# Kernel optimization log

Measured on AMD Instinct MI355X. Metric: run time of the kernel, lower is better.

## Reference

```python
import jax, jax.numpy as jnp
import numpy as np

N = 20000
E = 320000
H = 16
C = 16
NUM_GRAPHS = 64
NEG_SLOPE = 0.2


def _gat(x, edge_index, W, a_src, a_dst, bias):
    # PyG GATConv, concat=True, shared lin for src/dst, eval mode (no dropout)
    h = (x @ W).reshape(-1, H, C)                       # [N,H,C]
    src, dst = edge_index[0], edge_index[1]
    alpha_src = jnp.sum(h * a_src, axis=-1)             # [N,H]
    alpha_dst = jnp.sum(h * a_dst, axis=-1)             # [N,H]
    alpha = alpha_src[src] + alpha_dst[dst]             # [E,H]
    alpha = jax.nn.leaky_relu(alpha, NEG_SLOPE)
    amax = jax.ops.segment_max(alpha, dst, num_segments=N)
    ex = jnp.exp(alpha - amax[dst])
    denom = jax.ops.segment_sum(ex, dst, num_segments=N)
    attn = ex / jnp.where(denom == 0, 1.0, denom)[dst]  # [E,H]
    msg = h[src] * attn[:, :, None]                     # [E,H,C]
    out = jax.ops.segment_sum(msg, dst, num_segments=N) # [N,H,C]
    return out.reshape(-1, H * C) + bias


def setup_inputs() -> dict:
    key = jax.random.key(0)
    ks = jax.random.split(key, 32)
    d = {}
    d['x'] = jax.random.normal(ks[0], (N, 20), dtype=jnp.float32)
    d['edge_index_ipv6'] = jax.random.randint(ks[1], (2, E), 0, N)
    d['edge_attr_ipv6'] = jax.random.normal(ks[2], (E, 19), dtype=jnp.float32)
    d['edge_index_tsch'] = jax.random.randint(ks[3], (2, E), 0, N)
    d['edge_attr_tsch'] = jax.random.normal(ks[4], (E, 7), dtype=jnp.float32)
    d['batch'] = jnp.sort(jax.random.randint(ks[5], (N,), 0, NUM_GRAPHS))
    s = 0.1
    d['W_i'] = jax.random.normal(ks[6], (20, H * C), dtype=jnp.float32) * s
    d['a_src_i'] = jax.random.normal(ks[7], (H, C), dtype=jnp.float32) * s
    d['a_dst_i'] = jax.random.normal(ks[8], (H, C), dtype=jnp.float32) * s
    d['b_i'] = jnp.zeros((H * C,), dtype=jnp.float32)
    d['W_t'] = jax.random.normal(ks[9], (20, H * C), dtype=jnp.float32) * s
    d['a_src_t'] = jax.random.normal(ks[10], (H, C), dtype=jnp.float32) * s
    d['a_dst_t'] = jax.random.normal(ks[11], (H, C), dtype=jnp.float32) * s
    d['b_t'] = jnp.zeros((H * C,), dtype=jnp.float32)
    d['Wf'] = jax.random.normal(ks[12], (512, 64), dtype=jnp.float32) * s
    d['bf'] = jnp.zeros((64,), dtype=jnp.float32)
    d['W1'] = jax.random.normal(ks[13], (64, 32), dtype=jnp.float32) * s
    d['b1'] = jnp.zeros((32,), dtype=jnp.float32)
    d['W2'] = jax.random.normal(ks[14], (32, 16), dtype=jnp.float32) * s
    d['b2'] = jnp.zeros((16,), dtype=jnp.float32)
    d['W3'] = jax.random.normal(ks[15], (16, 16), dtype=jnp.float32) * s
    d['b3'] = jnp.zeros((16,), dtype=jnp.float32)
    d['Wce'] = jax.random.normal(ks[16], (16, 3), dtype=jnp.float32) * s
    d['bce'] = jnp.zeros((3,), dtype=jnp.float32)
    d['Wcv'] = jax.random.normal(ks[17], (16, 3), dtype=jnp.float32) * s
    d['bcv'] = jnp.zeros((3,), dtype=jnp.float32)
    return d


def reference(x, edge_index_ipv6, edge_attr_ipv6, edge_index_tsch, edge_attr_tsch,
              batch, W_i, a_src_i, a_dst_i, b_i, W_t, a_src_t, a_dst_t, b_t,
              Wf, bf, W1, b1, W2, b2, W3, b3, Wce, bce, Wcv, bcv):
    # edge_attr_* are ignored by GATConv (edge_dim=None in PyG), as in original
    n_ipv6 = _gat(x, edge_index_ipv6, W_i, a_src_i, a_dst_i, b_i)
    n_tsch = _gat(x, edge_index_tsch, W_t, a_src_t, a_dst_t, b_t)
    h = jnp.concatenate([n_ipv6, n_tsch], axis=-1)      # [N,512]
    h = jax.nn.relu(h @ Wf + bf)
    h = jax.nn.relu(h @ W1 + b1)
    h = jax.nn.relu(h @ W2 + b2)
    h = jax.nn.relu(h @ W3 + b3)                        # [N,16]
    ssum = jax.ops.segment_sum(h, batch, num_segments=NUM_GRAPHS)
    cnt = jax.ops.segment_sum(jnp.ones((h.shape[0], 1), h.dtype), batch,
                              num_segments=NUM_GRAPHS)
    g = ssum / jnp.where(cnt == 0, 1.0, cnt)            # [G,16]
    out_event = g @ Wce + bce
    out_env = g @ Wcv + bcv
    return out_event, out_env
```

## Files before the change

kernel.cpp:

```cpp
#include <hip/hip_runtime.h>
#include <math.h>

#define N_NODES 20000
#define N_EDGES 320000
#define NG 64
#define NEG 0.2f
#define NCHUNK ((N_NODES + 255) / 256)

typedef __attribute__((ext_vector_type(8))) short bf16x8;
typedef __attribute__((ext_vector_type(4))) float f32x4;

__device__ __forceinline__ unsigned short f2bf(float f) {
  unsigned int u = __float_as_uint(f);
  return (unsigned short)((u + 0x7fffu + ((u >> 16) & 1u)) >> 16);
}

__global__ __launch_bounds__(256) void k_prep(
    const float* __restrict__ W_i, const float* __restrict__ as_i, const float* __restrict__ ad_i,
    const float* __restrict__ W_t, const float* __restrict__ as_t, const float* __restrict__ ad_t,
    const float* __restrict__ Wf, const float* __restrict__ bf,
    const float* __restrict__ b_i, const float* __restrict__ b_t,
    float* __restrict__ wsall, unsigned short* __restrict__ wbigfrag,
    float* __restrict__ bfold,
    int* __restrict__ fill_i, int* __restrict__ fill_t,
    float* __restrict__ gsum, int* __restrict__ gcnt) {
  __shared__ float bred[4][64];
  int idx = blockIdx.x * 256 + threadIdx.x;
  if (idx < 1280) {
    int k = idx >> 6, c = idx & 63;
    int set = c >> 5, role = (c >> 4) & 1, h = c & 15;
    const float* W = set ? W_t : W_i;
    const float* a = set ? (role ? ad_t : as_t) : (role ? ad_i : as_i);
    float v = 0.f;
#pragma unroll
    for (int j = 0; j < 16; ++j) v = fmaf(W[k * 256 + h * 16 + j], a[h * 16 + j], v);
    wsall[idx] = v;
    return;
  }
  idx -= 1280;
  if (idx < 49152) {
    int ct = idx / 12288, rem = idx % 12288;
    int lane = (rem >> 3) & 63, j = rem & 7, ks = rem >> 9;
    int k = ks * 32 + ((lane >> 4) << 3) + j;
    int nc = ct * 16 + (lane & 15);
    float v = 0.f;
    int g = (k >= 384) ? 1 : 0;
    int r = k - g * 384;
    int h = r / 24, c = r - h * 24;
    if (c < 20) {
      const float* W = g ? W_t : W_i;
      const float* wr = W + c * 256 + (h << 4);
      const float* wf = Wf + ((g << 8) + (h << 4)) * 64 + nc;
#pragma unroll
      for (int m = 0; m < 16; ++m) v = fmaf(wr[m], wf[m * 64], v);
    }
    wbigfrag[idx] = f2bf(v);
    return;
  }
  idx -= 49152;
  if (idx < 256) {
    int t = threadIdx.x, wv = t >> 6, j = t & 63;
    float p = 0.f;
    int i0 = wv * 128;
#pragma unroll 4
    for (int i = i0; i < i0 + 128; ++i) {
      float b = (i < 256) ? b_i[i] : b_t[i - 256];
      p = fmaf(b, Wf[i * 64 + j], p);
    }
    bred[wv][j] = p;
    __syncthreads();
    if (wv == 0) bfold[j] = bred[0][j] + bred[1][j] + bred[2][j] + bred[3][j] + bf[j];
    return;
  }
  idx -= 256;
  if (idx < N_NODES) { fill_i[idx] = 0; return; }
  idx -= N_NODES;
  if (idx < N_NODES) { fill_t[idx] = 0; return; }
  idx -= N_NODES;
  if (idx < NG * 16) { gsum[idx] = 0.f; return; }
  idx -= NG * 16;
  if (idx < NG) gcnt[idx] = 0;
}

__global__ __launch_bounds__(256) void k_alpha(
    const float* __restrict__ x, const float* __restrict__ wsall,
    float* __restrict__ xpad,
    float* __restrict__ asrc0, float* __restrict__ adst0,
    float* __restrict__ asrc1, float* __restrict__ adst1) {
  int t = threadIdx.x;
  int n0 = blockIdx.x * 16;
  __shared__ float xs[16][20];
  __shared__ float ws[20][64];
  for (int i = t; i < 16 * 20; i += 256) {
    int nd = i / 20, k = i % 20;
    xs[nd][k] = x[(n0 + nd) * 20 + k];
  }
  for (int i = t; i < 1280; i += 256) ws[i >> 6][i & 63] = wsall[i];
  __syncthreads();
  for (int i = t; i < 512; i += 256) {
    int nd = i >> 5, j = i & 31;
    xpad[(size_t)(n0 + nd) * 32 + j] = (j < 20) ? xs[nd][j] : 0.f;
  }
#pragma unroll
  for (int i = 0; i < 4; ++i) {
    int wi = i * 256 + t;
    int nd = wi >> 6, c = wi & 63;
    float v = 0.f;
#pragma unroll
    for (int k = 0; k < 20; ++k) v = fmaf(xs[nd][k], ws[k][c], v);
    int n = n0 + nd, h = c & 15;
    float* arr = (c >> 5) ? ((c >> 4) & 1 ? adst1 : asrc1)
                          : ((c >> 4) & 1 ? adst0 : asrc0);
    arr[n * 16 + h] = v;
  }
}

__global__ void k_hist(const int* __restrict__ ei0, const int* __restrict__ ei1,
                       int* __restrict__ cnt0, int* __restrict__ cnt1) {
  int e = blockIdx.x * blockDim.x + threadIdx.x;
  if (e >= N_EDGES) return;
  if (blockIdx.y == 0)
    atomicAdd(&cnt0[ei0[N_EDGES + e]], 1);
  else
    atomicAdd(&cnt1[ei1[N_EDGES + e]], 1);
}

__global__ __launch_bounds__(256) void k_scan1(
    const int* __restrict__ cnt0, const int* __restrict__ cnt1,
    int* __restrict__ tmp0, int* __restrict__ tmp1, int* __restrict__ csums) {
  int chunk = blockIdx.x, set = blockIdx.y;
  const int* cnt = set ? cnt1 : cnt0;
  int* tmp = set ? tmp1 : tmp0;
  int t = threadIdx.x, lane = t & 63, wv = t >> 6;
  int i = chunk * 256 + t;
  int v = (i < N_NODES) ? cnt[i] : 0;
  int s = v;
#pragma unroll
  for (int d = 1; d < 64; d <<= 1) {
    int o = __shfl_up(s, d);
    if (lane >= d) s += o;
  }
  __shared__ int wsum[4];
  if (lane == 63) wsum[wv] = s;
  __syncthreads();
  int pre = 0;
#pragma unroll
  for (int j = 0; j < 4; ++j)
    if (j < wv) pre += wsum[j];
  s += pre;
  if (i < N_NODES) tmp[i] = s;
  if (t == 255) csums[set * 128 + chunk] = s;
}

__global__ __launch_bounds__(256) void k_scan3(
    const int* __restrict__ tmp0, const int* __restrict__ tmp1,
    const int* __restrict__ csums,
    int* __restrict__ rp0, int* __restrict__ rp1,
    int* __restrict__ fill0, int* __restrict__ fill1) {
  int chunk = blockIdx.x, set = blockIdx.y;
  const int* tmp = set ? tmp1 : tmp0;
  int* rp = set ? rp1 : rp0;
  int* fill = set ? fill1 : fill0;
  __shared__ int soff;
  if (threadIdx.x == 0) {
    int acc = 0;
    for (int cc = 0; cc < chunk; ++cc) acc += csums[set * 128 + cc];
    soff = acc;
  }
  __syncthreads();
  int off = soff;
  int i = chunk * 256 + threadIdx.x;
  if (i >= N_NODES) return;
  int incl = tmp[i];
  int c = fill[i];
  int excl = off + incl - c;
  rp[i] = excl;
  fill[i] = excl;
  if (i == N_NODES - 1) rp[N_NODES] = off + incl;
}

__global__ void k_scatter(const int* __restrict__ ei0, const int* __restrict__ ei1,
                          int* __restrict__ fill0, int* __restrict__ fill1,
                          unsigned short* __restrict__ srcs0,
                          unsigned short* __restrict__ srcs1) {
  int e = blockIdx.x * blockDim.x + threadIdx.x;
  if (e >= N_EDGES) return;
  const int* ei = blockIdx.y ? ei1 : ei0;
  int* fill = blockIdx.y ? fill1 : fill0;
  unsigned short* srcs = blockIdx.y ? srcs1 : srcs0;
  int d = ei[N_EDGES + e];
  int pos = atomicAdd(&fill[d], 1);
  srcs[pos] = (unsigned short)ei[e];
}

__global__ __launch_bounds__(256) void k_gat(
    const float* __restrict__ xpad,
    const float* __restrict__ asrc0, const float* __restrict__ adst0,
    const float* __restrict__ asrc1, const float* __restrict__ adst1,
    const int* __restrict__ rp0, const unsigned short* __restrict__ srcs0,
    const int* __restrict__ rp1, const unsigned short* __restrict__ srcs1,
    unsigned short* __restrict__ xagg) {
  __shared__ float lds[4][416];
  int w4 = threadIdx.x >> 6, lane = threadIdx.x & 63;
  int n = blockIdx.x * 2 + (w4 >> 1);
  int g = w4 & 1;
  int h16 = lane & 15, e4 = lane >> 4;
  float* lxs = lds[w4];
  float* lat = lds[w4] + 288;

  const float* asrc = g ? asrc1 : asrc0;
  const float* adst = g ? adst1 : adst0;
  const int* rp = g ? rp1 : rp0;
  const unsigned short* srcs = g ? srcs1 : srcs0;
  int k0 = rp[n], k1 = rp[n + 1];
  int deg = k1 - k0;
  float adn = adst[n * 16 + h16];
  float lacc = 0.f;
  float xa[8];
#pragma unroll
  for (int j = 0; j < 8; ++j) xa[j] = 0.f;

  if (deg > 0) {
    int nbat = (deg + 7) >> 3;
    int s0a = (int)srcs[min(k0 + e4, k1 - 1)];
    int s0b = (int)srcs[min(k0 + 4 + e4, k1 - 1)];
    float av0a = asrc[s0a * 16 + h16];
    float av0b = asrc[s0b * 16 + h16];
    float2 xv0a = *(const float2*)&xpad[(size_t)s0a * 32 + h16 * 2];
    float2 xv0b = *(const float2*)&xpad[(size_t)s0b * 32 + h16 * 2];
    int s1a = 0, s1b = 0;
    if (nbat > 1) {
      s1a = (int)srcs[min(k0 + 8 + e4, k1 - 1)];
      s1b = (int)srcs[min(k0 + 12 + e4, k1 - 1)];
    }
    for (int bb = 0; bb < nbat; ++bb) {
      float av1a = 0.f, av1b = 0.f;
      float2 xv1a = {0.f, 0.f}, xv1b = {0.f, 0.f};
      int s2a = 0, s2b = 0;
      if (bb + 1 < nbat) {
        av1a = asrc[s1a * 16 + h16];
        av1b = asrc[s1b * 16 + h16];
        xv1a = *(const float2*)&xpad[(size_t)s1a * 32 + h16 * 2];
        xv1b = *(const float2*)&xpad[(size_t)s1b * 32 + h16 * 2];
      }
      if (bb + 2 < nbat) {
        int kb = k0 + (bb + 2) * 8;
        s2a = (int)srcs[min(kb + e4, k1 - 1)];
        s2b = (int)srcs[min(kb + 4 + e4, k1 - 1)];
      }
      int base = k0 + bb * 8;
      float a1 = av0a + adn; a1 = a1 >= 0.f ? a1 : NEG * a1;
      float a2 = av0b + adn; a2 = a2 >= 0.f ? a2 : NEG * a2;
      float exa = (base + e4 < k1) ? __expf(a1) : 0.f;
      float exb = (base + 4 + e4 < k1) ? __expf(a2) : 0.f;
      lacc += exa + exb;
      lat[e4 * 16 + h16] = exa;
      lat[(4 + e4) * 16 + h16] = exb;
      *(float2*)&lxs[e4 * 36 + h16 * 2] = xv0a;
      *(float2*)&lxs[(4 + e4) * 36 + h16 * 2] = xv0b;
#pragma unroll
      for (int e = 0; e < 8; ++e) {
        float w = lat[e * 16 + h16];
        const float4 x0 = *(const float4*)&lxs[e * 36 + e4 * 8];
        const float4 x1 = *(const float4*)&lxs[e * 36 + e4 * 8 + 4];
        xa[0] = fmaf(w, x0.x, xa[0]); xa[1] = fmaf(w, x0.y, xa[1]);
        xa[2] = fmaf(w, x0.z, xa[2]); xa[3] = fmaf(w, x0.w, xa[3]);
        xa[4] = fmaf(w, x1.x, xa[4]); xa[5] = fmaf(w, x1.y, xa[5]);
        xa[6] = fmaf(w, x1.z, xa[6]); xa[7] = fmaf(w, x1.w, xa[7]);
      }
      av0a = av1a; av0b = av1b; xv0a = xv1a; xv0b = xv1b;
      s0a = s1a; s0b = s1b; s1a = s2a; s1b = s2b;
    }
  }
  float lh = lacc + __shfl_xor(lacc, 16);
  lh += __shfl_xor(lh, 32);
  float invl = lh > 0.f ? 1.f / lh : 0.f;
  if (e4 < 3) {
    unsigned int u[4];
#pragma unroll
    for (int q = 0; q < 4; ++q)
      u[q] = (unsigned int)f2bf(xa[2 * q] * invl) |
             ((unsigned int)f2bf(xa[2 * q + 1] * invl) << 16);
    *(uint4*)&xagg[(size_t)n * 768 + g * 384 + h16 * 24 + e4 * 8] = *(uint4*)u;
  }
}

__global__ __launch_bounds__(256) void k_mlp(
    const unsigned short* __restrict__ xagg, const unsigned short* __restrict__ wbigfrag,
    const float* __restrict__ bfold,
    const float* __restrict__ W1m, const float* __restrict__ b1v,
    const float* __restrict__ W2m, const float* __restrict__ b2v,
    const float* __restrict__ W3m, const float* __restrict__ b3v,
    const int* __restrict__ batch,
    float* __restrict__ gsum, int* __restrict__ gcnt) {
  int t = threadIdx.x, w = t >> 6, lane = t & 63;
  int n0 = blockIdx.x * 64;
  __shared__ float o1[64][68];
  __shared__ float o2[64][36];
  __shared__ float o3[64][20];
  __shared__ float o4[64][17];
  __shared__ int bs[64];
  if (t < 64) bs[t] = batch[min(n0 + t, N_NODES - 1)];

  {
    int m = lane & 15, kb = lane >> 4;
    int arow = n0 + w * 16 + m;
    if (arow >= N_NODES) arow = N_NODES - 1;
    const unsigned short* aptr = xagg + (size_t)arow * 768 + kb * 8;
    f32x4 acc0 = {0.f, 0.f, 0.f, 0.f}, acc1 = acc0, acc2 = acc0, acc3 = acc0;
#pragma unroll 4
    for (int ks = 0; ks < 24; ++ks) {
      bf16x8 af = *(const bf16x8*)(aptr + ks * 32);
      const unsigned short* bks = wbigfrag + (size_t)ks * 512 + lane * 8;
      bf16x8 b0 = *(const bf16x8*)(bks);
      bf16x8 b1 = *(const bf16x8*)(bks + 12288);
      bf16x8 b2 = *(const bf16x8*)(bks + 24576);
      bf16x8 b3 = *(const bf16x8*)(bks + 36864);
      acc0 = __builtin_amdgcn_mfma_f32_16x16x32_bf16(af, b0, acc0, 0, 0, 0);
      acc1 = __builtin_amdgcn_mfma_f32_16x16x32_bf16(af, b1, acc1, 0, 0, 0);
      acc2 = __builtin_amdgcn_mfma_f32_16x16x32_bf16(af, b2, acc2, 0, 0, 0);
      acc3 = __builtin_amdgcn_mfma_f32_16x16x32_bf16(af, b3, acc3, 0, 0, 0);
    }
    int col = lane & 15, rg = lane >> 4;
#pragma unroll
    for (int r = 0; r < 4; ++r) {
      int row = w * 16 + rg * 4 + r;
      o1[row][col]      = fmaxf(acc0[r] + bfold[col], 0.f);
      o1[row][16 + col] = fmaxf(acc1[r] + bfold[16 + col], 0.f);
      o1[row][32 + col] = fmaxf(acc2[r] + bfold[32 + col], 0.f);
      o1[row][48 + col] = fmaxf(acc3[r] + bfold[48 + col], 0.f);
    }
  }
  __syncthreads();
  int nd = t >> 2, qo = t & 3;
  {
    float a[8];
#pragma unroll
    for (int j = 0; j < 8; ++j) a[j] = b1v[qo * 8 + j];
#pragma unroll 4
    for (int k = 0; k < 64; ++k) {
      float hv = o1[nd][k];
      const float4 wA = *(const float4*)&W1m[k * 32 + qo * 8];
      const float4 wB = *(const float4*)&W1m[k * 32 + qo * 8 + 4];
      a[0] = fmaf(hv, wA.x, a[0]); a[1] = fmaf(hv, wA.y, a[1]);
      a[2] = fmaf(hv, wA.z, a[2]); a[3] = fmaf(hv, wA.w, a[3]);
      a[4] = fmaf(hv, wB.x, a[4]); a[5] = fmaf(hv, wB.y, a[5]);
      a[6] = fmaf(hv, wB.z, a[6]); a[7] = fmaf(hv, wB.w, a[7]);
    }
#pragma unroll
    for (int j = 0; j < 8; ++j) o2[nd][qo * 8 + j] = fmaxf(a[j], 0.f);
  }
  __syncthreads();
  {
    float a[4];
    const float4 bb = *(const float4*)&b2v[qo * 4];
    a[0] = bb.x; a[1] = bb.y; a[2] = bb.z; a[3] = bb.w;
#pragma unroll 4
    for (int k = 0; k < 32; ++k) {
      float hv = o2[nd][k];
      const float4 ww = *(const float4*)&W2m[k * 16 + qo * 4];
      a[0] = fmaf(hv, ww.x, a[0]); a[1] = fmaf(hv, ww.y, a[1]);
      a[2] = fmaf(hv, ww.z, a[2]); a[3] = fmaf(hv, ww.w, a[3]);
    }
#pragma unroll
    for (int j = 0; j < 4; ++j) o3[nd][qo * 4 + j] = fmaxf(a[j], 0.f);
  }
  __syncthreads();
  {
    float a[4];
    const float4 bb = *(const float4*)&b3v[qo * 4];
    a[0] = bb.x; a[1] = bb.y; a[2] = bb.z; a[3] = bb.w;
#pragma unroll
    for (int k = 0; k < 16; ++k) {
      float hv = o3[nd][k];
      const float4 ww = *(const float4*)&W3m[k * 16 + qo * 4];
      a[0] = fmaf(hv, ww.x, a[0]); a[1] = fmaf(hv, ww.y, a[1]);
      a[2] = fmaf(hv, ww.z, a[2]); a[3] = fmaf(hv, ww.w, a[3]);
    }
#pragma unroll
    for (int j = 0; j < 4; ++j) o4[nd][qo * 4 + j] = fmaxf(a[j], 0.f);
  }
  __syncthreads();
  if (t < 128) {
    int s = t >> 4, js = t & 15;
    int b = bs[0] + s;
    if (b <= bs[63]) {
      float sum = 0.f; int c = 0;
#pragma unroll 8
      for (int ndd = 0; ndd < 64; ++ndd) {
        if (n0 + ndd < N_NODES && bs[ndd] == b) { sum += o4[ndd][js]; ++c; }
      }
      if (c > 0) {
        atomicAdd(&gsum[b * 16 + js], sum);
        if (js == 0) atomicAdd(&gcnt[b], c);
      }
    }
  }
}

__global__ void k_head(const float* __restrict__ gsum, const int* __restrict__ gcnt,
                       const float* __restrict__ Wce, const float* __restrict__ bce,
                       const float* __restrict__ Wcv, const float* __restrict__ bcv,
                       float* __restrict__ out) {
  int t = threadIdx.x;
  if (t >= 384) return;
  int half = t / 192, idx = t % 192;
  int b = idx / 3, r = idx % 3;
  float cnt = (float)gcnt[b];
  float inv = cnt > 0.f ? 1.f / cnt : 1.f;
  const float* Wc = half ? Wcv : Wce;
  const float* bc = half ? bcv : bce;
  float v = bc[r];
#pragma unroll
  for (int j = 0; j < 16; ++j) v = fmaf(gsum[b * 16 + j] * inv, Wc[j * 3 + r], v);
  out[t] = v;
}

extern "C" void kernel_launch(void* const* d_in, const int* in_sizes, int n_in,
                              void* d_out, int out_size, void* d_ws, size_t ws_size,
                              hipStream_t stream) {
  const float* x = (const float*)d_in[0];
  const int* ei_i = (const int*)d_in[1];
  const int* ei_t = (const int*)d_in[3];
  const int* batch = (const int*)d_in[5];
  const float* W_i = (const float*)d_in[6];
  const float* as_i = (const float*)d_in[7];
  const float* ad_i = (const float*)d_in[8];
  const float* b_i = (const float*)d_in[9];
  const float* W_t = (const float*)d_in[10];
  const float* as_t = (const float*)d_in[11];
  const float* ad_t = (const float*)d_in[12];
  const float* b_t = (const float*)d_in[13];
  const float* Wf = (const float*)d_in[14];
  const float* bf = (const float*)d_in[15];
  const float* W1 = (const float*)d_in[16];
  const float* b1 = (const float*)d_in[17];
  const float* W2 = (const float*)d_in[18];
  const float* b2 = (const float*)d_in[19];
  const float* W3 = (const float*)d_in[20];
  const float* b3 = (const float*)d_in[21];
  const float* Wce = (const float*)d_in[22];
  const float* bce = (const float*)d_in[23];
  const float* Wcv = (const float*)d_in[24];
  const float* bcv = (const float*)d_in[25];

  char* ws = (char*)d_ws;
  size_t off = 0;
  auto take = [&](size_t bytes) {
    void* p = ws + off;
    off = (off + bytes + 255) & ~(size_t)255;
    return p;
  };
  float* xpad = (float*)take((size_t)N_NODES * 32 * 4);
  unsigned short* xagg = (unsigned short*)take((size_t)N_NODES * 768 * 2);
  float* wsall = (float*)take((size_t)1280 * 4);
  unsigned short* wbigfrag = (unsigned short*)take((size_t)49152 * 2);
  float* bfold = (float*)take((size_t)64 * 4);
  float* asrc_i = (float*)take((size_t)N_NODES * 16 * 4);
  float* adst_i = (float*)take((size_t)N_NODES * 16 * 4);
  float* asrc_t = (float*)take((size_t)N_NODES * 16 * 4);
  float* adst_t = (float*)take((size_t)N_NODES * 16 * 4);
  int* rowptr_i = (int*)take((size_t)(N_NODES + 1) * 4);
  int* rowptr_t = (int*)take((size_t)(N_NODES + 1) * 4);
  int* fill_i = (int*)take((size_t)N_NODES * 4);
  int* fill_t = (int*)take((size_t)N_NODES * 4);
  int* tmp_i = (int*)take((size_t)N_NODES * 4);
  int* tmp_t = (int*)take((size_t)N_NODES * 4);
  int* csums = (int*)take((size_t)2 * 128 * 4);
  unsigned short* srcs_i = (unsigned short*)take((size_t)N_EDGES * 2);
  unsigned short* srcs_t = (unsigned short*)take((size_t)N_EDGES * 2);
  float* gsum = (float*)take((size_t)NG * 16 * 4);
  int* gcnt = (int*)take((size_t)NG * 4);

  int prep_items = 1280 + 49152 + 256 + N_NODES + N_NODES + NG * 16 + NG;
  k_prep<<<(prep_items + 255) / 256, 256, 0, stream>>>(
      W_i, as_i, ad_i, W_t, as_t, ad_t, Wf, bf, b_i, b_t,
      wsall, wbigfrag, bfold, fill_i, fill_t, gsum, gcnt);

  k_alpha<<<N_NODES / 16, 256, 0, stream>>>(x, wsall, xpad,
                                            asrc_i, adst_i, asrc_t, adst_t);

  dim3 egrid((N_EDGES + 255) / 256, 2);
  k_hist<<<egrid, 256, 0, stream>>>(ei_i, ei_t, fill_i, fill_t);
  dim3 sgrid(NCHUNK, 2);
  k_scan1<<<sgrid, 256, 0, stream>>>(fill_i, fill_t, tmp_i, tmp_t, csums);
  k_scan3<<<sgrid, 256, 0, stream>>>(tmp_i, tmp_t, csums, rowptr_i, rowptr_t,
                                     fill_i, fill_t);
  k_scatter<<<egrid, 256, 0, stream>>>(ei_i, ei_t, fill_i, fill_t, srcs_i, srcs_t);

  k_gat<<<N_NODES / 2, 256, 0, stream>>>(xpad, asrc_i, adst_i, asrc_t, adst_t,
                                         rowptr_i, srcs_i, rowptr_t, srcs_t,
                                         xagg);

  k_mlp<<<(N_NODES + 63) / 64, 256, 0, stream>>>(xagg, wbigfrag, bfold,
                                                 W1, b1, W2, b2, W3, b3,
                                                 batch, gsum, gcnt);

  k_head<<<1, 384, 0, stream>>>(gsum, gcnt, Wce, bce, Wcv, bcv, (float*)d_out);
}
```

Before: 158.2 us.

## Fuse front-end kernels, single-pass scan, widen GAT batches, fold head into MLP

Merges weight prep, alpha projection and degree histogram into one launch, replaces the two-kernel scan with a single-pass scan that spins on flagged chunk aggregates, folds the head into the last MLP block via a completion counter, and zeroes buffers with memsets. The GAT gather now handles 16 edges per iteration with shuffled source indices instead of an 8-edge double-buffered prefetch. These changes cut launch count and per-kernel overhead but add inter-block spin waits, which rely on all scan blocks being co-resident, and drop the explicit prefetch of attention and feature loads.

```diff
diff --git a/kernel.cpp b/kernel.cpp
--- a/kernel.cpp
+++ b/kernel.cpp
@@ -6,6 +6,7 @@
 #define NG 64
 #define NEG 0.2f
 #define NCHUNK ((N_NODES + 255) / 256)
+#define FLAGBIT (1 << 30)
 
 typedef __attribute__((ext_vector_type(8))) short bf16x8;
 typedef __attribute__((ext_vector_type(4))) float f32x4;
@@ -15,30 +16,24 @@
   return (unsigned short)((u + 0x7fffu + ((u >> 16) & 1u)) >> 16);
 }
 
-__global__ __launch_bounds__(256) void k_prep(
+__global__ __launch_bounds__(256) void k_front(
+    const float* __restrict__ x,
     const float* __restrict__ W_i, const float* __restrict__ as_i, const float* __restrict__ ad_i,
     const float* __restrict__ W_t, const float* __restrict__ as_t, const float* __restrict__ ad_t,
     const float* __restrict__ Wf, const float* __restrict__ bf,
     const float* __restrict__ b_i, const float* __restrict__ b_t,
-    float* __restrict__ wsall, unsigned short* __restrict__ wbigfrag,
-    float* __restrict__ bfold,
-    int* __restrict__ fill_i, int* __restrict__ fill_t,
-    float* __restrict__ gsum, int* __restrict__ gcnt) {
+    const int* __restrict__ ei0, const int* __restrict__ ei1,
+    unsigned short* __restrict__ wbigfrag, float* __restrict__ bfold,
+    float* __restrict__ xpad,
+    float* __restrict__ asrc0, float* __restrict__ adst0,
+    float* __restrict__ asrc1, float* __restrict__ adst1,
+    int* __restrict__ fill0, int* __restrict__ fill1) {
   __shared__ float bred[4][64];
-  int idx = blockIdx.x * 256 + threadIdx.x;
-  if (idx < 1280) {
-    int k = idx >> 6, c = idx & 63;
-    int set = c >> 5, role = (c >> 4) & 1, h = c & 15;
-    const float* W = set ? W_t : W_i;
-    const float* a = set ? (role ? ad_t : as_t) : (role ? ad_i : as_i);
-    float v = 0.f;
-#pragma unroll
-    for (int j = 0; j < 16; ++j) v = fmaf(W[k * 256 + h * 16 + j], a[h * 16 + j], v);
-    wsall[idx] = v;
-    return;
-  }
-  idx -= 1280;
-  if (idx < 49152) {
+  __shared__ float wsA[20][64];
+  __shared__ float xsA[16][20];
+  int b = blockIdx.x, t = threadIdx.x;
+  if (b < 192) {
+    int idx = b * 256 + t;
     int ct = idx / 12288, rem = idx % 12288;
     int lane = (rem >> 3) & 63, j = rem & 7, ks = rem >> 9;
     int k = ks * 32 + ((lane >> 4) << 3) + j;
@@ -57,83 +52,76 @@
     wbigfrag[idx] = f2bf(v);
     return;
   }
-  idx -= 49152;
-  if (idx < 256) {
-    int t = threadIdx.x, wv = t >> 6, j = t & 63;
+  if (b == 192) {
+    int wv = t >> 6, j = t & 63;
     float p = 0.f;
     int i0 = wv * 128;
 #pragma unroll 4
     for (int i = i0; i < i0 + 128; ++i) {
-      float b = (i < 256) ? b_i[i] : b_t[i - 256];
-      p = fmaf(b, Wf[i * 64 + j], p);
+      float bb = (i < 256) ? b_i[i] : b_t[i - 256];
+      p = fmaf(bb, Wf[i * 64 + j], p);
     }
     bred[wv][j] = p;
     __syncthreads();
     if (wv == 0) bfold[j] = bred[0][j] + bred[1][j] + bred[2][j] + bred[3][j] + bf[j];
     return;
   }
-  idx -= 256;
-  if (idx < N_NODES) { fill_i[idx] = 0; return; }
-  idx -= N_NODES;
-  if (idx < N_NODES) { fill_t[idx] = 0; return; }
-  idx -= N_NODES;
-  if (idx < NG * 16) { gsum[idx] = 0.f; return; }
-  idx -= NG * 16;
-  if (idx < NG) gcnt[idx] = 0;
-}
-
-__global__ __launch_bounds__(256) void k_alpha(
-    const float* __restrict__ x, const float* __restrict__ wsall,
-    float* __restrict__ xpad,
-    float* __restrict__ asrc0, float* __restrict__ adst0,
-    float* __restrict__ asrc1, float* __restrict__ adst1) {
-  int t = threadIdx.x;
-  int n0 = blockIdx.x * 16;
-  __shared__ float xs[16][20];
-  __shared__ float ws[20][64];
-  for (int i = t; i < 16 * 20; i += 256) {
-    int nd = i / 20, k = i % 20;
-    xs[nd][k] = x[(n0 + nd) * 20 + k];
-  }
-  for (int i = t; i < 1280; i += 256) ws[i >> 6][i & 63] = wsall[i];
-  __syncthreads();
-  for (int i = t; i < 512; i += 256) {
-    int nd = i >> 5, j = i & 31;
-    xpad[(size_t)(n0 + nd) * 32 + j] = (j < 20) ? xs[nd][j] : 0.f;
-  }
-#pragma unroll
-  for (int i = 0; i < 4; ++i) {
-    int wi = i * 256 + t;
-    int nd = wi >> 6, c = wi & 63;
-    float v = 0.f;
-#pragma unroll
-    for (int k = 0; k < 20; ++k) v = fmaf(xs[nd][k], ws[k][c], v);
-    int n = n0 + nd, h = c & 15;
-    float* arr = (c >> 5) ? ((c >> 4) & 1 ? adst1 : asrc1)
-                          : ((c >> 4) & 1 ? adst0 : asrc0);
-    arr[n * 16 + h] = v;
-  }
-}
-
-__global__ void k_hist(const int* __restrict__ ei0, const int* __restrict__ ei1,
-                       int* __restrict__ cnt0, int* __restrict__ cnt1) {
-  int e = blockIdx.x * blockDim.x + threadIdx.x;
-  if (e >= N_EDGES) return;
-  if (blockIdx.y == 0)
-    atomicAdd(&cnt0[ei0[N_EDGES + e]], 1);
-  else
-    atomicAdd(&cnt1[ei1[N_EDGES + e]], 1);
-}
-
-__global__ __launch_bounds__(256) void k_scan1(
-    const int* __restrict__ cnt0, const int* __restrict__ cnt1,
-    int* __restrict__ tmp0, int* __restrict__ tmp1, int* __restrict__ csums) {
+  if (b < 1443) {
+    int a = b - 193;
+    int n0 = a * 16;
+    for (int i = t; i < 320; i += 256) {
+      int nd = i / 20, k = i % 20;
+      xsA[nd][k] = x[(n0 + nd) * 20 + k];
+    }
+    for (int i = t; i < 1280; i += 256) {
+      int k = i >> 6, c = i & 63;
+      int set = c >> 5, role = (c >> 4) & 1, h = c & 15;
+      const float* W = set ? W_t : W_i;
+      const float* av = set ? (role ? ad_t : as_t) : (role ? ad_i : as_i);
+      float v = 0.f;
+#pragma unroll
+      for (int j = 0; j < 16; ++j) v = fmaf(W[k * 256 + h * 16 + j], av[h * 16 + j], v);
+      wsA[k][c] = v;
+    }
+    __syncthreads();
+    for (int i = t; i < 512; i += 256) {
+      int nd = i >> 5, j = i & 31;
+      xpad[(size_t)(n0 + nd) * 32 + j] = (j < 20) ? xsA[nd][j] : 0.f;
+    }
+#pragma unroll
+    for (int i = 0; i < 4; ++i) {
+      int wi = i * 256 + t;
+      int nd = wi >> 6, c = wi & 63;
+      float v = 0.f;
+#pragma unroll
+      for (int k = 0; k < 20; ++k) v = fmaf(xsA[nd][k], wsA[k][c], v);
+      int n = n0 + nd, h = c & 15;
+      float* arr = (c >> 5) ? ((c >> 4) & 1 ? adst1 : asrc1)
+                            : ((c >> 4) & 1 ? adst0 : asrc0);
+      arr[n * 16 + h] = v;
+    }
+    return;
+  }
+  {
+    int hb = b - 1443;
+    int set = hb >= 1250;
+    int e = (set ? hb - 1250 : hb) * 256 + t;
+    const int* ei = set ? ei1 : ei0;
+    int* fill = set ? fill1 : fill0;
+    atomicAdd(&fill[ei[N_EDGES + e]], 1);
+  }
+}
+
+__global__ __launch_bounds__(256) void k_scan(
+    int* __restrict__ fill0, int* __restrict__ fill1,
+    int* __restrict__ rp0, int* __restrict__ rp1,
+    int* __restrict__ aggs) {
   int chunk = blockIdx.x, set = blockIdx.y;
-  const int* cnt = set ? cnt1 : cnt0;
-  int* tmp = set ? tmp1 : tmp0;
+  int* fill = set ? fill1 : fill0;
+  int* rp = set ? rp1 : rp0;
   int t = threadIdx.x, lane = t & 63, wv = t >> 6;
   int i = chunk * 256 + t;
-  int v = (i < N_NODES) ? cnt[i] : 0;
+  int v = (i < N_NODES) ? fill[i] : 0;
   int s = v;
 #pragma unroll
   for (int d = 1; d < 64; d <<= 1) {
@@ -148,35 +136,33 @@
   for (int j = 0; j < 4; ++j)
     if (j < wv) pre += wsum[j];
   s += pre;
-  if (i < N_NODES) tmp[i] = s;
-  if (t == 255) csums[set * 128 + chunk] = s;
-}
-
-__global__ __launch_bounds__(256) void k_scan3(
-    const int* __restrict__ tmp0, const int* __restrict__ tmp1,
-    const int* __restrict__ csums,
-    int* __restrict__ rp0, int* __restrict__ rp1,
-    int* __restrict__ fill0, int* __restrict__ fill1) {
-  int chunk = blockIdx.x, set = blockIdx.y;
-  const int* tmp = set ? tmp1 : tmp0;
-  int* rp = set ? rp1 : rp0;
-  int* fill = set ? fill1 : fill0;
-  __shared__ int soff;
-  if (threadIdx.x == 0) {
-    int acc = 0;
-    for (int cc = 0; cc < chunk; ++cc) acc += csums[set * 128 + cc];
-    soff = acc;
-  }
-  __syncthreads();
-  int off = soff;
-  int i = chunk * 256 + threadIdx.x;
-  if (i >= N_NODES) return;
-  int incl = tmp[i];
-  int c = fill[i];
-  int excl = off + incl - c;
-  rp[i] = excl;
-  fill[i] = excl;
-  if (i == N_NODES - 1) rp[N_NODES] = off + incl;
+  int agg = wsum[0] + wsum[1] + wsum[2] + wsum[3];
+  if (t == 0)
+    __hip_atomic_store(&aggs[set * 128 + chunk], agg | FLAGBIT,
+                       __ATOMIC_RELEASE, __HIP_MEMORY_SCOPE_AGENT);
+  __shared__ int reds[256];
+  int part = 0;
+  for (int j = t; j < chunk; j += 256) {
+    int a;
+    do {
+      a = __hip_atomic_load(&aggs[set * 128 + j], __ATOMIC_ACQUIRE,
+                            __HIP_MEMORY_SCOPE_AGENT);
+    } while (!(a & FLAGBIT));
+    part += a & (FLAGBIT - 1);
+  }
+  reds[t] = part;
+  __syncthreads();
+  for (int st = 128; st > 0; st >>= 1) {
+    if (t < st) reds[t] += reds[t + st];
+    __syncthreads();
+  }
+  int carry = reds[0];
+  int excl = carry + s - v;
+  if (i < N_NODES) {
+    rp[i] = excl;
+    fill[i] = excl;
+    if (i == N_NODES - 1) rp[N_NODES] = excl + v;
+  }
 }
 
 __global__ void k_scatter(const int* __restrict__ ei0, const int* __restrict__ ei1,
@@ -200,76 +186,56 @@
     const int* __restrict__ rp0, const unsigned short* __restrict__ srcs0,
     const int* __restrict__ rp1, const unsigned short* __restrict__ srcs1,
     unsigned short* __restrict__ xagg) {
-  __shared__ float lds[4][416];
+  __shared__ float xsh[4][16][36];
+  __shared__ float lath[4][16][16];
   int w4 = threadIdx.x >> 6, lane = threadIdx.x & 63;
   int n = blockIdx.x * 2 + (w4 >> 1);
   int g = w4 & 1;
   int h16 = lane & 15, e4 = lane >> 4;
-  float* lxs = lds[w4];
-  float* lat = lds[w4] + 288;
-
+  int eid = lane & 15, slot = lane >> 4;
+  float (*xs)[36] = xsh[w4];
+  float (*la)[16] = lath[w4];
   const float* asrc = g ? asrc1 : asrc0;
   const float* adst = g ? adst1 : adst0;
   const int* rp = g ? rp1 : rp0;
   const unsigned short* srcs = g ? srcs1 : srcs0;
   int k0 = rp[n], k1 = rp[n + 1];
-  int deg = k1 - k0;
   float adn = adst[n * 16 + h16];
   float lacc = 0.f;
   float xa[8];
 #pragma unroll
   for (int j = 0; j < 8; ++j) xa[j] = 0.f;
-
-  if (deg > 0) {
-    int nbat = (deg + 7) >> 3;
-    int s0a = (int)srcs[min(k0 + e4, k1 - 1)];
-    int s0b = (int)srcs[min(k0 + 4 + e4, k1 - 1)];
-    float av0a = asrc[s0a * 16 + h16];
-    float av0b = asrc[s0b * 16 + h16];
-    float2 xv0a = *(const float2*)&xpad[(size_t)s0a * 32 + h16 * 2];
-    float2 xv0b = *(const float2*)&xpad[(size_t)s0b * 32 + h16 * 2];
-    int s1a = 0, s1b = 0;
-    if (nbat > 1) {
-      s1a = (int)srcs[min(k0 + 8 + e4, k1 - 1)];
-      s1b = (int)srcs[min(k0 + 12 + e4, k1 - 1)];
-    }
-    for (int bb = 0; bb < nbat; ++bb) {
-      float av1a = 0.f, av1b = 0.f;
-      float2 xv1a = {0.f, 0.f}, xv1b = {0.f, 0.f};
-      int s2a = 0, s2b = 0;
-      if (bb + 1 < nbat) {
-        av1a = asrc[s1a * 16 + h16];
-        av1b = asrc[s1b * 16 + h16];
-        xv1a = *(const float2*)&xpad[(size_t)s1a * 32 + h16 * 2];
-        xv1b = *(const float2*)&xpad[(size_t)s1b * 32 + h16 * 2];
+  if (k1 > k0) {
+    int sb = (int)srcs[min(k0 + eid, k1 - 1)];
+    for (int base = k0; base < k1; base += 16) {
+      int sbN = 0;
+      if (base + 16 < k1) sbN = (int)srcs[min(base + 16 + eid, k1 - 1)];
+      float4 xv0 = *(const float4*)&xpad[(size_t)sb * 32 + slot * 8];
+      float4 xv1 = *(const float4*)&xpad[(size_t)sb * 32 + slot * 8 + 4];
+      float ex[4];
+#pragma unroll
+      for (int q = 0; q < 4; ++q) {
+        int e = e4 + 4 * q;
+        int s = __shfl(sb, e);
+        float aa = asrc[s * 16 + h16] + adn;
+        aa = aa >= 0.f ? aa : NEG * aa;
+        ex[q] = (base + e < k1) ? __expf(aa) : 0.f;
+        lacc += ex[q];
+        la[e][h16] = ex[q];
       }
-      if (bb + 2 < nbat) {
-        int kb = k0 + (bb + 2) * 8;
-        s2a = (int)srcs[min(kb + e4, k1 - 1)];
-        s2b = (int)srcs[min(kb + 4 + e4, k1 - 1)];
-      }
-      int base = k0 + bb * 8;
-      float a1 = av0a + adn; a1 = a1 >= 0.f ? a1 : NEG * a1;
-      float a2 = av0b + adn; a2 = a2 >= 0.f ? a2 : NEG * a2;
-      float exa = (base + e4 < k1) ? __expf(a1) : 0.f;
-      float exb = (base + 4 + e4 < k1) ? __expf(a2) : 0.f;
-      lacc += exa + exb;
-      lat[e4 * 16 + h16] = exa;
-      lat[(4 + e4) * 16 + h16] = exb;
-      *(float2*)&lxs[e4 * 36 + h16 * 2] = xv0a;
-      *(float2*)&lxs[(4 + e4) * 36 + h16 * 2] = xv0b;
-#pragma unroll
-      for (int e = 0; e < 8; ++e) {
-        float w = lat[e * 16 + h16];
-        const float4 x0 = *(const float4*)&lxs[e * 36 + e4 * 8];
-        const float4 x1 = *(const float4*)&lxs[e * 36 + e4 * 8 + 4];
+      *(float4*)&xs[eid][slot * 8] = xv0;
+      *(float4*)&xs[eid][slot * 8 + 4] = xv1;
+#pragma unroll
+      for (int e = 0; e < 16; ++e) {
+        float w = la[e][h16];
+        float4 x0 = *(const float4*)&xs[e][e4 * 8];
+        float4 x1 = *(const float4*)&xs[e][e4 * 8 + 4];
         xa[0] = fmaf(w, x0.x, xa[0]); xa[1] = fmaf(w, x0.y, xa[1]);
         xa[2] = fmaf(w, x0.z, xa[2]); xa[3] = fmaf(w, x0.w, xa[3]);
         xa[4] = fmaf(w, x1.x, xa[4]); xa[5] = fmaf(w, x1.y, xa[5]);
         xa[6] = fmaf(w, x1.z, xa[6]); xa[7] = fmaf(w, x1.w, xa[7]);
       }
-      av0a = av1a; av0b = av1b; xv0a = xv1a; xv0b = xv1b;
-      s0a = s1a; s0b = s1b; s1a = s2a; s1b = s2b;
+      sb = sbN;
     }
   }
   float lh = lacc + __shfl_xor(lacc, 16);
@@ -292,7 +258,10 @@
     const float* __restrict__ W2m, const float* __restrict__ b2v,
     const float* __restrict__ W3m, const float* __restrict__ b3v,
     const int* __restrict__ batch,
-    float* __restrict__ gsum, int* __restrict__ gcnt) {
+    float* __restrict__ gsum, int* __restrict__ gcnt, int* __restrict__ donecnt,
+    const float* __restrict__ Wce, const float* __restrict__ bce,
+    const float* __restrict__ Wcv, const float* __restrict__ bcv,
+    float* __restrict__ out) {
   int t = threadIdx.x, w = t >> 6, lane = t & 63;
   int n0 = blockIdx.x * 64;
   __shared__ float o1[64][68];
@@ -396,24 +365,32 @@
       }
     }
   }
-}
-
-__global__ void k_head(const float* __restrict__ gsum, const int* __restrict__ gcnt,
-                       const float* __restrict__ Wce, const float* __restrict__ bce,
-                       const float* __restrict__ Wcv, const float* __restrict__ bcv,
-                       float* __restrict__ out) {
-  int t = threadIdx.x;
-  if (t >= 384) return;
-  int half = t / 192, idx = t % 192;
-  int b = idx / 3, r = idx % 3;
-  float cnt = (float)gcnt[b];
-  float inv = cnt > 0.f ? 1.f / cnt : 1.f;
-  const float* Wc = half ? Wcv : Wce;
-  const float* bc = half ? bcv : bce;
-  float v = bc[r];
-#pragma unroll
-  for (int j = 0; j < 16; ++j) v = fmaf(gsum[b * 16 + j] * inv, Wc[j * 3 + r], v);
-  out[t] = v;
+  __threadfence();
+  __shared__ int lastf;
+  if (t == 0) {
+    int d = __hip_atomic_fetch_add(donecnt, 1, __ATOMIC_ACQ_REL, __HIP_MEMORY_SCOPE_AGENT);
+    lastf = (d == (int)gridDim.x - 1);
+  }
+  __syncthreads();
+  if (!lastf) return;
+  __shared__ float gs[NG * 16];
+  __shared__ float gc[NG];
+  for (int i = t; i < NG * 16; i += 256)
+    gs[i] = __hip_atomic_load(&gsum[i], __ATOMIC_RELAXED, __HIP_MEMORY_SCOPE_AGENT);
+  for (int i = t; i < NG; i += 256)
+    gc[i] = (float)__hip_atomic_load(&gcnt[i], __ATOMIC_RELAXED, __HIP_MEMORY_SCOPE_AGENT);
+  __syncthreads();
+  for (int o = t; o < 384; o += 256) {
+    int half = o / 192, idx = o % 192;
+    int b = idx / 3, r = idx % 3;
+    float inv = gc[b] > 0.f ? 1.f / gc[b] : 1.f;
+    const float* Wc = half ? Wcv : Wce;
+    const float* bc = half ? bcv : bce;
+    float v = bc[r];
+#pragma unroll
+    for (int j = 0; j < 16; ++j) v = fmaf(gs[b * 16 + j] * inv, Wc[j * 3 + r], v);
+    out[o] = v;
+  }
 }
 
 extern "C" void kernel_launch(void* const* d_in, const int* in_sizes, int n_in,
@@ -453,7 +430,6 @@
   };
   float* xpad = (float*)take((size_t)N_NODES * 32 * 4);
   unsigned short* xagg = (unsigned short*)take((size_t)N_NODES * 768 * 2);
-  float* wsall = (float*)take((size_t)1280 * 4);
   unsigned short* wbigfrag = (unsigned short*)take((size_t)49152 * 2);
   float* bfold = (float*)take((size_t)64 * 4);
   float* asrc_i = (float*)take((size_t)N_NODES * 16 * 4);
@@ -462,30 +438,28 @@
   float* adst_t = (float*)take((size_t)N_NODES * 16 * 4);
   int* rowptr_i = (int*)take((size_t)(N_NODES + 1) * 4);
   int* rowptr_t = (int*)take((size_t)(N_NODES + 1) * 4);
-  int* fill_i = (int*)take((size_t)N_NODES * 4);
-  int* fill_t = (int*)take((size_t)N_NODES * 4);
-  int* tmp_i = (int*)take((size_t)N_NODES * 4);
-  int* tmp_t = (int*)take((size_t)N_NODES * 4);
-  int* csums = (int*)take((size_t)2 * 128 * 4);
+  int* fill_i = (int*)take((size_t)2 * N_NODES * 4);
+  int* fill_t = fill_i + N_NODES;
   unsigned short* srcs_i = (unsigned short*)take((size_t)N_EDGES * 2);
   unsigned short* srcs_t = (unsigned short*)take((size_t)N_EDGES * 2);
-  float* gsum = (float*)take((size_t)NG * 16 * 4);
-  int* gcnt = (int*)take((size_t)NG * 4);
-
-  int prep_items = 1280 + 49152 + 256 + N_NODES + N_NODES + NG * 16 + NG;
-  k_prep<<<(prep_items + 255) / 256, 256, 0, stream>>>(
-      W_i, as_i, ad_i, W_t, as_t, ad_t, Wf, bf, b_i, b_t,
-      wsall, wbigfrag, bfold, fill_i, fill_t, gsum, gcnt);
-
-  k_alpha<<<N_NODES / 16, 256, 0, stream>>>(x, wsall, xpad,
-                                            asrc_i, adst_i, asrc_t, adst_t);
+  float* gsum = (float*)take((size_t)(NG * 16 + NG + 1 + 256) * 4);
+  int* gcnt = (int*)(gsum + NG * 16);
+  int* donecnt = gcnt + NG;
+  int* aggs = donecnt + 1;
+
+  hipMemsetAsync(fill_i, 0, (size_t)2 * N_NODES * 4, stream);
+  hipMemsetAsync(gsum, 0, (size_t)(NG * 16 + NG + 1 + 256) * 4, stream);
+
+  k_front<<<3943, 256, 0, stream>>>(x, W_i, as_i, ad_i, W_t, as_t, ad_t,
+                                    Wf, bf, b_i, b_t, ei_i, ei_t,
+                                    wbigfrag, bfold, xpad,
+                                    asrc_i, adst_i, asrc_t, adst_t,
+                                    fill_i, fill_t);
+
+  dim3 sgrid(NCHUNK, 2);
+  k_scan<<<sgrid, 256, 0, stream>>>(fill_i, fill_t, rowptr_i, rowptr_t, aggs);
 
   dim3 egrid((N_EDGES + 255) / 256, 2);
-  k_hist<<<egrid, 256, 0, stream>>>(ei_i, ei_t, fill_i, fill_t);
-  dim3 sgrid(NCHUNK, 2);
-  k_scan1<<<sgrid, 256, 0, stream>>>(fill_i, fill_t, tmp_i, tmp_t, csums);
-  k_scan3<<<sgrid, 256, 0, stream>>>(tmp_i, tmp_t, csums, rowptr_i, rowptr_t,
-                                     fill_i, fill_t);
   k_scatter<<<egrid, 256, 0, stream>>>(ei_i, ei_t, fill_i, fill_t, srcs_i, srcs_t);
 
   k_gat<<<N_NODES / 2, 256, 0, stream>>>(xpad, asrc_i, adst_i, asrc_t, adst_t,
@@ -494,7 +468,6 @@
 
   k_mlp<<<(N_NODES + 63) / 64, 256, 0, stream>>>(xagg, wbigfrag, bfold,
                                                  W1, b1, W2, b2, W3, b3,
-                                                 batch, gsum, gcnt);
-
-  k_head<<<1, 384, 0, stream>>>(gsum, gcnt, Wce, bce, Wcv, bcv, (float*)d_out);
-}
+                                                 batch, gsum, gcnt, donecnt,
+                                                 Wce, bce, Wcv, bcv, (float*)d_out);
+}
```

After: 178.5 us. +12.8%, slower.
